# Performance work log

Hardware: AMD Instinct MI355X
Metric: run time of the kernel (lower is better)

## Reference

```python
import jax, jax.numpy as jnp
import numpy as np

N_NODES = 50000
N_EDGES = 800000
IN_DIM = 128
OUT_DIM = 64
K_KERNELS = 2
S_ATTEN = 2


def setup_inputs() -> dict:
    key = jax.random.key(0)
    ks = jax.random.split(key, 9)
    return {
        "x": jax.random.normal(ks[0], (N_NODES, IN_DIM), dtype=jnp.float32),
        "support_vals": jax.random.uniform(ks[1], (K_KERNELS, N_EDGES), dtype=jnp.float32),
        "atten_vals": jax.random.uniform(ks[2], (S_ATTEN, N_EDGES), dtype=jnp.float32),
        "W_transform": jax.random.normal(ks[3], (K_KERNELS, IN_DIM, OUT_DIM), dtype=jnp.float32) * 0.05,
        "w_left": jax.random.normal(ks[4], (K_KERNELS, S_ATTEN + 1, OUT_DIM), dtype=jnp.float32) * 0.05,
        "w_right": jax.random.normal(ks[5], (K_KERNELS, S_ATTEN + 1, OUT_DIM), dtype=jnp.float32) * 0.05,
        "W_residual": jax.random.normal(ks[6], (IN_DIM + OUT_DIM, OUT_DIM), dtype=jnp.float32) * 0.05,
        "edge_rows": jax.random.randint(ks[7], (N_EDGES,), 0, N_NODES, dtype=jnp.int64),
        "edge_cols": jax.random.randint(ks[8], (N_EDGES,), 0, N_NODES, dtype=jnp.int64),
    }


def reference(x, support_vals, atten_vals, W_transform, w_left, w_right, W_residual, edge_rows, edge_cols):
    # x: [N, F], edge lists: [E]; all supports share the same sparsity pattern.
    N = x.shape[0]
    K = W_transform.shape[0]
    output = jnp.zeros((N, W_transform.shape[2]), dtype=x.dtype)
    for k in range(K):
        wx = x @ W_transform[k]                       # [N, D]
        al = wx @ w_left[k].T                         # [N, S+1]
        ar = wx @ w_right[k].T                        # [N, S+1]
        # per-support edge values; support i=S uses this kernel's Cheb support
        vals = jnp.concatenate([atten_vals, support_vals[k][None, :]], axis=0)  # [S+1, E]
        # score_e = sum_i (al[row_e,i] + ar[col_e,i]) * vals[i,e]
        scores = jnp.einsum('es,se->e', al[edge_rows] + ar[edge_cols], vals)    # [E]
        # row-wise (segment) softmax over nonzeros, as tf.sparse_softmax
        m = jax.ops.segment_max(scores, edge_rows, num_segments=N)              # [N]
        ex = jnp.exp(scores - m[edge_rows])
        denom = jax.ops.segment_sum(ex, edge_rows, num_segments=N)              # [N]
        probs = ex / denom[edge_rows]                                           # [E]
        # spmm: out[r] = sum_{e: row_e=r} probs_e * wx[col_e]
        output = output + jax.ops.segment_sum(probs[:, None] * wx[edge_cols], edge_rows, num_segments=N)
    # residual projection then elu activation
    output = jnp.concatenate([x, output], axis=-1) @ W_residual
    return jax.nn.elu(output)
```

## Files before the change

### kernel.cpp

```cpp
#include <hip/hip_runtime.h>

#define N_NODES 50000
#define N_EDGES 800000
#define IN_DIM 128
#define OUT_DIM 64
#define NEG_INF (-1e30f)
#define GBLK ((N_NODES + 63) / 64)
#define BSHIFT 7
#define NBUK ((N_NODES + 127) >> 7)
#define EB 1024
#define PREB ((N_EDGES + EB - 1) / EB)
#define NFRAG (3 * 16 + 8)
#define STAGE_CAP 3072

typedef unsigned short ushort_t;
typedef __attribute__((ext_vector_type(8))) short short8;
typedef __attribute__((ext_vector_type(4))) float f32x4;

__device__ __forceinline__ unsigned f2bf(float f) {
    unsigned u = __float_as_uint(f);
    u += 0x7fffu + ((u >> 16) & 1u);
    return u >> 16;
}
__device__ __forceinline__ unsigned rl_u(unsigned v, int i) {
    return __builtin_amdgcn_readlane(v, i);
}
__device__ __forceinline__ float rl_f(float v, int i) {
    return __uint_as_float(__builtin_amdgcn_readlane(__float_as_uint(v), i));
}

__global__ void wpack_kernel(const float* __restrict__ Wt,
                             const float* __restrict__ Wres,
                             ushort_t* __restrict__ Wpack) {
    int idx = blockIdx.x * 256 + threadIdx.x;
    if (idx >= NFRAG * 512) return;
    int f = idx >> 9;
    int within = idx & 511;
    int lane = within >> 3;
    int b = within & 7;
    float val;
    if (f < 48) {
        int mat = f >> 4;
        int ct = (f >> 2) & 3;
        int kc = f & 3;
        int k = kc * 32 + (lane >> 4) * 8 + b;
        int c = ct * 16 + (lane & 15);
        const float* W = (mat < 2) ? (Wt + (size_t)mat * IN_DIM * OUT_DIM) : Wres;
        val = W[(size_t)k * OUT_DIM + c];
    } else {
        int f2 = f - 48;
        int ct = f2 >> 1;
        int kc = f2 & 1;
        int k = kc * 32 + (lane >> 4) * 8 + b;
        int c = ct * 16 + (lane & 15);
        val = Wres[(size_t)(IN_DIM + k) * OUT_DIM + c];
    }
    Wpack[idx] = (ushort_t)f2bf(val);
}

__global__ __launch_bounds__(256) void gemm_kernel(
        const float* __restrict__ x,
        const ushort_t* __restrict__ Wpack,
        const float* __restrict__ wl,
        const float* __restrict__ wr,
        unsigned* __restrict__ wxi,
        float* __restrict__ xres,
        float* __restrict__ al,
        float* __restrict__ ar) {
    int wave = threadIdx.x >> 6;
    int lane = threadIdx.x & 63;
    int lr = lane & 15;
    int lg = lane >> 4;
    int row0 = blockIdx.x * 64 + wave * 16;

    int arow = row0 + lr;
    if (arow >= N_NODES) arow = N_NODES - 1;
    const float* xr = x + (size_t)arow * IN_DIM;
    short8 afrag[4];
#pragma unroll
    for (int kc = 0; kc < 4; ++kc) {
        float4 f0 = *(const float4*)(xr + kc * 32 + lg * 8);
        float4 f1 = *(const float4*)(xr + kc * 32 + lg * 8 + 4);
        short8 a;
        a[0] = (short)f2bf(f0.x); a[1] = (short)f2bf(f0.y);
        a[2] = (short)f2bf(f0.z); a[3] = (short)f2bf(f0.w);
        a[4] = (short)f2bf(f1.x); a[5] = (short)f2bf(f1.y);
        a[6] = (short)f2bf(f1.z); a[7] = (short)f2bf(f1.w);
        afrag[kc] = a;
    }

    f32x4 acc[3][4] = {};
#pragma unroll
    for (int kc = 0; kc < 4; ++kc) {
#pragma unroll
        for (int mat = 0; mat < 3; ++mat) {
#pragma unroll
            for (int ct = 0; ct < 4; ++ct) {
                short8 bfrag = *(const short8*)(
                    Wpack + (size_t)(((mat * 4 + ct) * 4 + kc) << 9) + lane * 8);
                acc[mat][ct] = __builtin_amdgcn_mfma_f32_16x16x32_bf16(
                    afrag[kc], bfrag, acc[mat][ct], 0, 0, 0);
            }
        }
    }

#pragma unroll
    for (int r = 0; r < 4; ++r) {
        int gr = row0 + lg * 4 + r;
        if (gr < N_NODES) {
#pragma unroll
            for (int ct = 0; ct < 4; ++ct) {
                unsigned pk = f2bf(acc[0][ct][r]) | (f2bf(acc[1][ct][r]) << 16);
                wxi[(size_t)gr * OUT_DIM + ct * 16 + lr] = pk;
                xres[(size_t)gr * OUT_DIM + ct * 16 + lr] = acc[2][ct][r];
            }
        }
    }

#pragma unroll
    for (int mat = 0; mat < 2; ++mat) {
#pragma unroll
        for (int s = 0; s < 3; ++s) {
            float wlv[4], wrv[4];
#pragma unroll
            for (int ct = 0; ct < 4; ++ct) {
                wlv[ct] = wl[(size_t)(mat * 3 + s) * OUT_DIM + ct * 16 + lr];
                wrv[ct] = wr[(size_t)(mat * 3 + s) * OUT_DIM + ct * 16 + lr];
            }
#pragma unroll
            for (int r = 0; r < 4; ++r) {
                float pl = 0.f, pr = 0.f;
#pragma unroll
                for (int ct = 0; ct < 4; ++ct) {
                    pl = fmaf(acc[mat][ct][r], wlv[ct], pl);
                    pr = fmaf(acc[mat][ct][r], wrv[ct], pr);
                }
#pragma unroll
                for (int off = 1; off < 16; off <<= 1) {
                    pl += __shfl_xor(pl, off);
                    pr += __shfl_xor(pr, off);
                }
                if (lr == 0) {
                    int gr = row0 + lg * 4 + r;
                    if (gr < N_NODES) {
                        al[(size_t)gr * 6 + mat * 3 + s] = pl;
                        ar[(size_t)gr * 6 + mat * 3 + s] = pr;
                    }
                }
            }
        }
    }
}

__global__ __launch_bounds__(256) void score_sort_kernel(
        const int* __restrict__ rows,
        const int* __restrict__ cols,
        const float* __restrict__ atten,
        const float* __restrict__ support,
        const float* __restrict__ al,
        const float* __restrict__ ar,
        uint4* __restrict__ etmp,
        int* __restrict__ cnt_T,
        int* __restrict__ loff_T) {
    __shared__ int cnt[512];
    __shared__ int cur[512];
    __shared__ int aux[256];
    __shared__ uint4 stage[EB];
    int t = threadIdx.x;
    cnt[t] = 0; cnt[t + 256] = 0;
    __syncthreads();
    int base0 = blockIdx.x * EB;
    int nval = min(EB, N_EDGES - base0);

    int r_[4], c_[4];
    float s0_[4], s1_[4];
#pragma unroll
    for (int i = 0; i < 4; ++i) {
        int e = base0 + i * 256 + t;
        bool v = e < N_EDGES;
        int r = v ? rows[e] : -1;
        int c = v ? cols[e] : 0;
        float sc0 = 0.f, sc1 = 0.f;
        if (v) {
            float a0 = atten[e], a1 = atten[N_EDGES + e];
            float sp0 = support[e], sp1 = support[N_EDGES + e];
            const float* A = al + (size_t)r * 6;
            const float* B = ar + (size_t)c * 6;
            sc0 = (A[0] + B[0]) * a0 + (A[1] + B[1]) * a1 + (A[2] + B[2]) * sp0;
            sc1 = (A[3] + B[3]) * a0 + (A[4] + B[4]) * a1 + (A[5] + B[5]) * sp1;
            atomicAdd(&cnt[r >> BSHIFT], 1);
        }
        r_[i] = r; c_[i] = c; s0_[i] = sc0; s1_[i] = sc1;
    }
    __syncthreads();
    int a0 = cnt[2 * t], a1 = cnt[2 * t + 1];
    int ps = a0 + a1;
    aux[t] = ps;
    __syncthreads();
    int val = ps;
    for (int off = 1; off < 256; off <<= 1) {
        int y = (t >= off) ? aux[t - off] : 0;
        __syncthreads();
        val += y; aux[t] = val;
        __syncthreads();
    }
    int e2 = val - ps;
    cur[2 * t] = e2;
    cur[2 * t + 1] = e2 + a0;
    int b = blockIdx.x;
    if (2 * t < NBUK)     { cnt_T[(2 * t) * PREB + b] = a0;     loff_T[(2 * t) * PREB + b] = e2; }
    if (2 * t + 1 < NBUK) { cnt_T[(2 * t + 1) * PREB + b] = a1; loff_T[(2 * t + 1) * PREB + b] = e2 + a0; }
    __syncthreads();
#pragma unroll
    for (int i = 0; i < 4; ++i) {
        if (r_[i] < 0) continue;
        int pos = atomicAdd(&cur[r_[i] >> BSHIFT], 1);
        uint4 pv;
        pv.x = (unsigned)c_[i] | ((unsigned)(r_[i] & 127) << 16);
        pv.y = __float_as_uint(s0_[i]);
        pv.z = __float_as_uint(s1_[i]);
        pv.w = 0u;
        stage[pos] = pv;
    }
    __syncthreads();
    for (int i = t; i < nval; i += 256)
        etmp[(size_t)base0 + i] = stage[i];
}

__global__ void colscan_kernel(const int* __restrict__ cnt_T,
                               int* __restrict__ btot) {
    __shared__ int sh[256];
    int k = blockIdx.x, t = threadIdx.x;
    int s = 0;
    for (int b = t; b < PREB; b += 256) s += cnt_T[(size_t)k * PREB + b];
    sh[t] = s;
    __syncthreads();
    for (int off = 128; off > 0; off >>= 1) {
        if (t < off) sh[t] += sh[t + off];
        __syncthreads();
    }
    if (t == 0) btot[k] = sh[0];
}

__global__ __launch_bounds__(256) void sortb_kernel(
        const int* __restrict__ cnt_T,
        const int* __restrict__ loff_T,
        const int* __restrict__ btot,
        const uint4* __restrict__ etmp,
        uint4* __restrict__ edata,
        int* __restrict__ row_ptr) {
    __shared__ uint4 stage[STAGE_CAP];
    __shared__ int rpos[PREB + 2];
    __shared__ int lloff[PREB];
    __shared__ int aux[256];
    __shared__ int bb[512];
    __shared__ int hist[128], rcur[128];
    int k = blockIdx.x, t = threadIdx.x;

    bb[t] = (t < NBUK) ? btot[t] : 0;
    bb[t + 256] = (t + 256 < NBUK) ? btot[t + 256] : 0;
    __syncthreads();
    int a0 = bb[2 * t], a1 = bb[2 * t + 1];
    int ps = a0 + a1;
    aux[t] = ps;
    __syncthreads();
    int val = ps;
    for (int off = 1; off < 256; off <<= 1) {
        int y = (t >= off) ? aux[t - off] : 0;
        __syncthreads();
        val += y; aux[t] = val;
        __syncthreads();
    }
    bb[2 * t] = val - ps;
    bb[2 * t + 1] = val - ps + a0;
    __syncthreads();
    int base = bb[k];

    for (int b = t; b < PREB; b += 256) {
        rpos[b] = cnt_T[(size_t)k * PREB + b];
        lloff[b] = loff_T[(size_t)k * PREB + b];
    }
    if (t < 128) hist[t] = 0;
    __syncthreads();
    int v[4];
    int idx4 = 4 * t;
#pragma unroll
    for (int i = 0; i < 4; ++i) v[i] = (idx4 + i < PREB) ? rpos[idx4 + i] : 0;
    __syncthreads();
    int s = 0;
#pragma unroll
    for (int i = 0; i < 4; ++i) { int tmp = v[i]; v[i] = s; s += tmp; }
    aux[t] = s;
    __syncthreads();
    int tv = s;
    for (int off = 1; off < 256; off <<= 1) {
        int y = (t >= off) ? aux[t - off] : 0;
        __syncthreads();
        tv += y; aux[t] = tv;
        __syncthreads();
    }
    int ofs = tv - s;
#pragma unroll
    for (int i = 0; i < 4; ++i)
        if (idx4 + i <= PREB) rpos[idx4 + i] = ofs + v[i];
    __syncthreads();
    int nb = rpos[PREB];

    for (int j = t; j < nb; j += 256) {
        int lo = 0, hi = PREB - 1;
        while (lo < hi) { int mid = (lo + hi + 1) >> 1; if (rpos[mid] <= j) lo = mid; else hi = mid - 1; }
        uint4 rec = etmp[(size_t)lo * EB + lloff[lo] + (j - rpos[lo])];
        if (j < STAGE_CAP) stage[j] = rec;
        atomicAdd(&hist[(rec.x >> 16) & 127], 1);
    }
    __syncthreads();
    int hv = (t < 128) ? hist[t] : 0;
    aux[t] = hv;
    __syncthreads();
    int hval = hv;
    for (int off = 1; off < 128; off <<= 1) {
        int y = (t >= off && t < 128) ? aux[t - off] : 0;
        __syncthreads();
        hval += y; aux[t] = hval;
        __syncthreads();
    }
    if (t < 128) {
        rcur[t] = hval - hv;
        int row = (k << BSHIFT) + t;
        if (row < N_NODES) row_ptr[row] = base + hval - hv;
    }
    if (k == NBUK - 1 && t == 0) row_ptr[N_NODES] = N_EDGES;
    __syncthreads();
    for (int j = t; j < nb; j += 256) {
        uint4 rec;
        if (j < STAGE_CAP) rec = stage[j];
        else {
            int lo = 0, hi = PREB - 1;
            while (lo < hi) { int mid = (lo + hi + 1) >> 1; if (rpos[mid] <= j) lo = mid; else hi = mid - 1; }
            rec = etmp[(size_t)lo * EB + lloff[lo] + (j - rpos[lo])];
        }
        int rl = (rec.x >> 16) & 127;
        int dst = atomicAdd(&rcur[rl], 1);
        edata[(size_t)base + dst] = rec;
    }
}

__global__ void attn_kernel(const int* __restrict__ row_ptr,
                            const uint4* __restrict__ edata,
                            const unsigned* __restrict__ wxi,
                            float* __restrict__ aacc) {
    int wid = blockIdx.x * 4 + (threadIdx.x >> 6);
    if (wid >= N_NODES) return;
    int lane = threadIdx.x & 63;
    int beg = row_ptr[wid], end = row_ptr[wid + 1];
    int deg = end - beg;
    float a = 0.f;

    if (deg > 0 && deg <= 64) {
        bool valid = lane < deg;
        uint4 ed = edata[valid ? beg + lane : beg];
        unsigned c = ed.x & 0xFFFFu;
        float sc0 = valid ? __uint_as_float(ed.y) : NEG_INF;
        float sc1 = valid ? __uint_as_float(ed.z) : NEG_INF;
        float m0 = sc0, m1 = sc1;
#pragma unroll
        for (int off = 32; off > 0; off >>= 1) {
            m0 = fmaxf(m0, __shfl_xor(m0, off));
            m1 = fmaxf(m1, __shfl_xor(m1, off));
        }
        float e0 = valid ? __expf(sc0 - m0) : 0.f;
        float e1 = valid ? __expf(sc1 - m1) : 0.f;
        float l0 = e0, l1 = e1;
#pragma unroll
        for (int off = 32; off > 0; off >>= 1) {
            l0 += __shfl_xor(l0, off);
            l1 += __shfl_xor(l1, off);
        }
        float p0 = e0 / l0;
        float p1 = e1 / l1;
        float a0 = 0.f, a1 = 0.f, a2 = 0.f, a3 = 0.f;
        int i = 0;
        for (; i + 4 <= deg; i += 4) {
            unsigned c0 = rl_u(c, i),     c1 = rl_u(c, i + 1);
            unsigned c2 = rl_u(c, i + 2), c3 = rl_u(c, i + 3);
            unsigned v0 = wxi[(size_t)c0 * OUT_DIM + lane];
            unsigned v1 = wxi[(size_t)c1 * OUT_DIM + lane];
            unsigned v2 = wxi[(size_t)c2 * OUT_DIM + lane];
            unsigned v3 = wxi[(size_t)c3 * OUT_DIM + lane];
            a0 = fmaf(rl_f(p0, i),     __uint_as_float(v0 << 16), a0);
            a0 = fmaf(rl_f(p1, i),     __uint_as_float(v0 & 0xffff0000u), a0);
            a1 = fmaf(rl_f(p0, i + 1), __uint_as_float(v1 << 16), a1);
            a1 = fmaf(rl_f(p1, i + 1), __uint_as_float(v1 & 0xffff0000u), a1);
            a2 = fmaf(rl_f(p0, i + 2), __uint_as_float(v2 << 16), a2);
            a2 = fmaf(rl_f(p1, i + 2), __uint_as_float(v2 & 0xffff0000u), a2);
            a3 = fmaf(rl_f(p0, i + 3), __uint_as_float(v3 << 16), a3);
            a3 = fmaf(rl_f(p1, i + 3), __uint_as_float(v3 & 0xffff0000u), a3);
        }
        for (; i < deg; ++i) {
            unsigned ci = rl_u(c, i);
            unsigned v = wxi[(size_t)ci * OUT_DIM + lane];
            a0 = fmaf(rl_f(p0, i), __uint_as_float(v << 16), a0);
            a0 = fmaf(rl_f(p1, i), __uint_as_float(v & 0xffff0000u), a0);
        }
        a = (a0 + a1) + (a2 + a3);
    } else if (deg > 64) {
        float m0 = NEG_INF, l0 = 0.f, m1 = NEG_INF, l1 = 0.f;
        for (int base = beg; base < end; base += 64) {
            int pos = base + lane;
            bool valid = pos < end;
            uint4 ed = edata[valid ? pos : beg];
            float sc0 = valid ? __uint_as_float(ed.y) : NEG_INF;
            float sc1 = valid ? __uint_as_float(ed.z) : NEG_INF;
            float cm0 = sc0, cm1 = sc1;
#pragma unroll
            for (int off = 32; off > 0; off >>= 1) {
                cm0 = fmaxf(cm0, __shfl_xor(cm0, off));
                cm1 = fmaxf(cm1, __shfl_xor(cm1, off));
            }
            float mn0 = fmaxf(m0, cm0), mn1 = fmaxf(m1, cm1);
            float e0 = valid ? __expf(sc0 - mn0) : 0.f;
            float e1 = valid ? __expf(sc1 - mn1) : 0.f;
#pragma unroll
            for (int off = 32; off > 0; off >>= 1) {
                e0 += __shfl_xor(e0, off);
                e1 += __shfl_xor(e1, off);
            }
            l0 = l0 * __expf(m0 - mn0) + e0;
            l1 = l1 * __expf(m1 - mn1) + e1;
            m0 = mn0; m1 = mn1;
        }
        float inv0 = 1.f / l0, inv1 = 1.f / l1;
        for (int base = beg; base < end; base += 64) {
            int pos = base + lane;
            bool valid = pos < end;
            uint4 ed = edata[valid ? pos : beg];
            unsigned c = ed.x & 0xFFFFu;
            float p0 = valid ? __expf(__uint_as_float(ed.y) - m0) * inv0 : 0.f;
            float p1 = valid ? __expf(__uint_as_float(ed.z) - m1) * inv1 : 0.f;
            int cnt = min(64, end - base);
            for (int i = 0; i < cnt; ++i) {
                unsigned ci = rl_u(c, i);
                unsigned v = wxi[(size_t)ci * OUT_DIM + lane];
                a = fmaf(rl_f(p0, i), __uint_as_float(v << 16), a);
                a = fmaf(rl_f(p1, i), __uint_as_float(v & 0xffff0000u), a);
            }
        }
    }
    aacc[(size_t)wid * OUT_DIM + lane] = a;
}

__global__ __launch_bounds__(256) void resid_kernel(
        const float* __restrict__ aacc,
        const float* __restrict__ xres,
        const ushort_t* __restrict__ Wpack,
        float* __restrict__ out) {
    int wave = threadIdx.x >> 6;
    int lane = threadIdx.x & 63;
    int lr = lane & 15;
    int lg = lane >> 4;
    int row0 = blockIdx.x * 64 + wave * 16;
    int arow = row0 + lr;
    if (arow >= N_NODES) arow = N_NODES - 1;
    const float* ap = aacc + (size_t)arow * OUT_DIM;
    short8 af[2];
#pragma unroll
    for (int kc = 0; kc < 2; ++kc) {
        float4 f0 = *(const float4*)(ap + kc * 32 + lg * 8);
        float4 f1 = *(const float4*)(ap + kc * 32 + lg * 8 + 4);
        short8 a;
        a[0] = (short)f2bf(f0.x); a[1] = (short)f2bf(f0.y);
        a[2] = (short)f2bf(f0.z); a[3] = (short)f2bf(f0.w);
        a[4] = (short)f2bf(f1.x); a[5] = (short)f2bf(f1.y);
        a[6] = (short)f2bf(f1.z); a[7] = (short)f2bf(f1.w);
        af[kc] = a;
    }
    f32x4 acc4[4] = {};
#pragma unroll
    for (int kc = 0; kc < 2; ++kc) {
#pragma unroll
        for (int ct = 0; ct < 4; ++ct) {
            short8 bfrag = *(const short8*)(
                Wpack + (size_t)((48 + ct * 2 + kc) << 9) + lane * 8);
            acc4[ct] = __builtin_amdgcn_mfma_f32_16x16x32_bf16(
                af[kc], bfrag, acc4[ct], 0, 0, 0);
        }
    }
#pragma unroll
    for (int r = 0; r < 4; ++r) {
        int gr = row0 + lg * 4 + r;
        if (gr < N_NODES) {
#pragma unroll
            for (int ct = 0; ct < 4; ++ct) {
                float v = acc4[ct][r] + xres[(size_t)gr * OUT_DIM + ct * 16 + lr];
                out[(size_t)gr * OUT_DIM + ct * 16 + lr] = (v > 0.f) ? v : expm1f(v);
            }
        }
    }
}

extern "C" void kernel_launch(void* const* d_in, const int* in_sizes, int n_in,
                              void* d_out, int out_size, void* d_ws, size_t ws_size,
                              hipStream_t stream) {
    const float* x       = (const float*)d_in[0];
    const float* support = (const float*)d_in[1];
    const float* atten   = (const float*)d_in[2];
    const float* Wt      = (const float*)d_in[3];
    const float* wl      = (const float*)d_in[4];
    const float* wr      = (const float*)d_in[5];
    const float* Wres    = (const float*)d_in[6];
    const int*   rows    = (const int*)d_in[7];
    const int*   cols    = (const int*)d_in[8];
    float* out = (float*)d_out;

    unsigned* wxi   = (unsigned*)d_ws;
    float* xres     = (float*)(wxi + (size_t)N_NODES * OUT_DIM);
    float* al       = xres + (size_t)N_NODES * OUT_DIM;
    float* ar       = al + (size_t)N_NODES * 6;
    uint4* etmp     = (uint4*)(ar + (size_t)N_NODES * 6);
    uint4* edata    = etmp + (size_t)N_EDGES;
    int*   row_ptr  = (int*)(edata + (size_t)N_EDGES);
    int*   cnt_T    = row_ptr + N_NODES + 4;
    int*   loff_T   = cnt_T + (size_t)NBUK * PREB;
    int*   btot     = loff_T + (size_t)NBUK * PREB;
    ushort_t* Wpack = (ushort_t*)(btot + NBUK + 4);
    float* aacc     = (float*)etmp;

    wpack_kernel<<<(NFRAG * 512 + 255) / 256, 256, 0, stream>>>(Wt, Wres, Wpack);
    gemm_kernel<<<GBLK, 256, 0, stream>>>(x, Wpack, wl, wr, wxi, xres, al, ar);
    score_sort_kernel<<<PREB, 256, 0, stream>>>(
        rows, cols, atten, support, al, ar, etmp, cnt_T, loff_T);
    colscan_kernel<<<NBUK, 256, 0, stream>>>(cnt_T, btot);
    sortb_kernel<<<NBUK, 256, 0, stream>>>(
        cnt_T, loff_T, btot, etmp, edata, row_ptr);
    attn_kernel<<<(N_NODES + 3) / 4, 256, 0, stream>>>(
        row_ptr, edata, wxi, aacc);
    resid_kernel<<<GBLK, 256, 0, stream>>>(aacc, xres, Wpack, out);
}
```

Before: 153.7 us.

## Interleave bucket counts, chunk sortb gather, widen attn unroll, store bf16 aggregate

Bucket counts and local offsets are packed into one block-major uint2 array, so score_sort writes are coalesced and a single load fetches both values. sortb now walks each pre-block's contiguous run instead of binary-searching per element. attn unrolls the neighbor gather to 8 independent loads with 8 accumulators for more memory-level parallelism. The aggregated output is stored as bf16 so resid reads half the bytes and skips conversion. The trade-offs are strided column reads in colscan/sortb, per-thread serial loops with uneven work in sortb, and higher register pressure in attn.

```diff
diff --git a/kernel.cpp b/kernel.cpp
--- a/kernel.cpp
+++ b/kernel.cpp
@@ -8,6 +8,7 @@
 #define GBLK ((N_NODES + 63) / 64)
 #define BSHIFT 7
 #define NBUK ((N_NODES + 127) >> 7)
+#define NBUKP 392
 #define EB 1024
 #define PREB ((N_EDGES + EB - 1) / EB)
 #define NFRAG (3 * 16 + 8)
@@ -160,8 +161,7 @@
         const float* __restrict__ al,
         const float* __restrict__ ar,
         uint4* __restrict__ etmp,
-        int* __restrict__ cnt_T,
-        int* __restrict__ loff_T) {
+        uint2* __restrict__ cl) {
     __shared__ int cnt[512];
     __shared__ int cur[512];
     __shared__ int aux[256];
@@ -207,9 +207,9 @@
     int e2 = val - ps;
     cur[2 * t] = e2;
     cur[2 * t + 1] = e2 + a0;
-    int b = blockIdx.x;
-    if (2 * t < NBUK)     { cnt_T[(2 * t) * PREB + b] = a0;     loff_T[(2 * t) * PREB + b] = e2; }
-    if (2 * t + 1 < NBUK) { cnt_T[(2 * t + 1) * PREB + b] = a1; loff_T[(2 * t + 1) * PREB + b] = e2 + a0; }
+    size_t cb = (size_t)blockIdx.x * NBUKP;
+    if (2 * t < NBUK)     cl[cb + 2 * t]     = make_uint2((unsigned)a0, (unsigned)e2);
+    if (2 * t + 1 < NBUK) cl[cb + 2 * t + 1] = make_uint2((unsigned)a1, (unsigned)(e2 + a0));
     __syncthreads();
 #pragma unroll
     for (int i = 0; i < 4; ++i) {
@@ -227,12 +227,12 @@
         etmp[(size_t)base0 + i] = stage[i];
 }
 
-__global__ void colscan_kernel(const int* __restrict__ cnt_T,
+__global__ void colscan_kernel(const uint2* __restrict__ cl,
                                int* __restrict__ btot) {
     __shared__ int sh[256];
     int k = blockIdx.x, t = threadIdx.x;
     int s = 0;
-    for (int b = t; b < PREB; b += 256) s += cnt_T[(size_t)k * PREB + b];
+    for (int b = t; b < PREB; b += 256) s += (int)cl[(size_t)b * NBUKP + k].x;
     sh[t] = s;
     __syncthreads();
     for (int off = 128; off > 0; off >>= 1) {
@@ -243,8 +243,7 @@
 }
 
 __global__ __launch_bounds__(256) void sortb_kernel(
-        const int* __restrict__ cnt_T,
-        const int* __restrict__ loff_T,
+        const uint2* __restrict__ cl,
         const int* __restrict__ btot,
         const uint4* __restrict__ etmp,
         uint4* __restrict__ edata,
@@ -277,8 +276,9 @@
     int base = bb[k];
 
     for (int b = t; b < PREB; b += 256) {
-        rpos[b] = cnt_T[(size_t)k * PREB + b];
-        lloff[b] = loff_T[(size_t)k * PREB + b];
+        uint2 v2 = cl[(size_t)b * NBUKP + k];
+        rpos[b] = (int)v2.x;
+        lloff[b] = (int)v2.y;
     }
     if (t < 128) hist[t] = 0;
     __syncthreads();
@@ -306,12 +306,17 @@
     __syncthreads();
     int nb = rpos[PREB];
 
-    for (int j = t; j < nb; j += 256) {
-        int lo = 0, hi = PREB - 1;
-        while (lo < hi) { int mid = (lo + hi + 1) >> 1; if (rpos[mid] <= j) lo = mid; else hi = mid - 1; }
-        uint4 rec = etmp[(size_t)lo * EB + lloff[lo] + (j - rpos[lo])];
-        if (j < STAGE_CAP) stage[j] = rec;
-        atomicAdd(&hist[(rec.x >> 16) & 127], 1);
+    for (int b = t; b < PREB; b += 256) {
+        int s0 = rpos[b];
+        int n = rpos[b + 1] - s0;
+        int lo = lloff[b];
+        const uint4* src = etmp + (size_t)b * EB + lo;
+        for (int i = 0; i < n; ++i) {
+            uint4 rec = src[i];
+            int j = s0 + i;
+            if (j < STAGE_CAP) stage[j] = rec;
+            atomicAdd(&hist[(rec.x >> 16) & 127], 1);
+        }
     }
     __syncthreads();
     int hv = (t < 128) ? hist[t] : 0;
@@ -348,7 +353,7 @@
 __global__ void attn_kernel(const int* __restrict__ row_ptr,
                             const uint4* __restrict__ edata,
                             const unsigned* __restrict__ wxi,
-                            float* __restrict__ aacc) {
+                            ushort_t* __restrict__ aacc) {
     int wid = blockIdx.x * 4 + (threadIdx.x >> 6);
     if (wid >= N_NODES) return;
     int lane = threadIdx.x & 63;
@@ -378,31 +383,28 @@
         }
         float p0 = e0 / l0;
         float p1 = e1 / l1;
-        float a0 = 0.f, a1 = 0.f, a2 = 0.f, a3 = 0.f;
+        float acc8[8] = {};
         int i = 0;
-        for (; i + 4 <= deg; i += 4) {
-            unsigned c0 = rl_u(c, i),     c1 = rl_u(c, i + 1);
-            unsigned c2 = rl_u(c, i + 2), c3 = rl_u(c, i + 3);
-            unsigned v0 = wxi[(size_t)c0 * OUT_DIM + lane];
-            unsigned v1 = wxi[(size_t)c1 * OUT_DIM + lane];
-            unsigned v2 = wxi[(size_t)c2 * OUT_DIM + lane];
-            unsigned v3 = wxi[(size_t)c3 * OUT_DIM + lane];
-            a0 = fmaf(rl_f(p0, i),     __uint_as_float(v0 << 16), a0);
-            a0 = fmaf(rl_f(p1, i),     __uint_as_float(v0 & 0xffff0000u), a0);
-            a1 = fmaf(rl_f(p0, i + 1), __uint_as_float(v1 << 16), a1);
-            a1 = fmaf(rl_f(p1, i + 1), __uint_as_float(v1 & 0xffff0000u), a1);
-            a2 = fmaf(rl_f(p0, i + 2), __uint_as_float(v2 << 16), a2);
-            a2 = fmaf(rl_f(p1, i + 2), __uint_as_float(v2 & 0xffff0000u), a2);
-            a3 = fmaf(rl_f(p0, i + 3), __uint_as_float(v3 << 16), a3);
-            a3 = fmaf(rl_f(p1, i + 3), __uint_as_float(v3 & 0xffff0000u), a3);
+        for (; i + 8 <= deg; i += 8) {
+            unsigned cc[8], vv[8];
+#pragma unroll
+            for (int j = 0; j < 8; ++j) cc[j] = rl_u(c, i + j);
+#pragma unroll
+            for (int j = 0; j < 8; ++j) vv[j] = wxi[(size_t)cc[j] * OUT_DIM + lane];
+#pragma unroll
+            for (int j = 0; j < 8; ++j) {
+                acc8[j] = fmaf(rl_f(p0, i + j), __uint_as_float(vv[j] << 16), acc8[j]);
+                acc8[j] = fmaf(rl_f(p1, i + j), __uint_as_float(vv[j] & 0xffff0000u), acc8[j]);
+            }
         }
         for (; i < deg; ++i) {
             unsigned ci = rl_u(c, i);
             unsigned v = wxi[(size_t)ci * OUT_DIM + lane];
-            a0 = fmaf(rl_f(p0, i), __uint_as_float(v << 16), a0);
-            a0 = fmaf(rl_f(p1, i), __uint_as_float(v & 0xffff0000u), a0);
-        }
-        a = (a0 + a1) + (a2 + a3);
+            acc8[0] = fmaf(rl_f(p0, i), __uint_as_float(v << 16), acc8[0]);
+            acc8[0] = fmaf(rl_f(p1, i), __uint_as_float(v & 0xffff0000u), acc8[0]);
+        }
+        a = ((acc8[0] + acc8[1]) + (acc8[2] + acc8[3]))
+          + ((acc8[4] + acc8[5]) + (acc8[6] + acc8[7]));
     } else if (deg > 64) {
         float m0 = NEG_INF, l0 = 0.f, m1 = NEG_INF, l1 = 0.f;
         for (int base = beg; base < end; base += 64) {
@@ -446,11 +448,11 @@
             }
         }
     }
-    aacc[(size_t)wid * OUT_DIM + lane] = a;
+    aacc[(size_t)wid * OUT_DIM + lane] = (ushort_t)f2bf(a);
 }
 
 __global__ __launch_bounds__(256) void resid_kernel(
-        const float* __restrict__ aacc,
+        const ushort_t* __restrict__ aacc,
         const float* __restrict__ xres,
         const ushort_t* __restrict__ Wpack,
         float* __restrict__ out) {
@@ -461,19 +463,11 @@
     int row0 = blockIdx.x * 64 + wave * 16;
     int arow = row0 + lr;
     if (arow >= N_NODES) arow = N_NODES - 1;
-    const float* ap = aacc + (size_t)arow * OUT_DIM;
+    const ushort_t* ap = aacc + (size_t)arow * OUT_DIM;
     short8 af[2];
 #pragma unroll
-    for (int kc = 0; kc < 2; ++kc) {
-        float4 f0 = *(const float4*)(ap + kc * 32 + lg * 8);
-        float4 f1 = *(const float4*)(ap + kc * 32 + lg * 8 + 4);
-        short8 a;
-        a[0] = (short)f2bf(f0.x); a[1] = (short)f2bf(f0.y);
-        a[2] = (short)f2bf(f0.z); a[3] = (short)f2bf(f0.w);
-        a[4] = (short)f2bf(f1.x); a[5] = (short)f2bf(f1.y);
-        a[6] = (short)f2bf(f1.z); a[7] = (short)f2bf(f1.w);
-        af[kc] = a;
-    }
+    for (int kc = 0; kc < 2; ++kc)
+        af[kc] = *(const short8*)(ap + kc * 32 + lg * 8);
     f32x4 acc4[4] = {};
 #pragma unroll
     for (int kc = 0; kc < 2; ++kc) {
@@ -519,19 +513,18 @@
     uint4* etmp     = (uint4*)(ar + (size_t)N_NODES * 6);
     uint4* edata    = etmp + (size_t)N_EDGES;
     int*   row_ptr  = (int*)(edata + (size_t)N_EDGES);
-    int*   cnt_T    = row_ptr + N_NODES + 4;
-    int*   loff_T   = cnt_T + (size_t)NBUK * PREB;
-    int*   btot     = loff_T + (size_t)NBUK * PREB;
+    uint2* cl       = (uint2*)(row_ptr + N_NODES + 4);
+    int*   btot     = (int*)(cl + (size_t)PREB * NBUKP);
     ushort_t* Wpack = (ushort_t*)(btot + NBUK + 4);
-    float* aacc     = (float*)etmp;
+    ushort_t* aacc  = (ushort_t*)etmp;
 
     wpack_kernel<<<(NFRAG * 512 + 255) / 256, 256, 0, stream>>>(Wt, Wres, Wpack);
     gemm_kernel<<<GBLK, 256, 0, stream>>>(x, Wpack, wl, wr, wxi, xres, al, ar);
     score_sort_kernel<<<PREB, 256, 0, stream>>>(
-        rows, cols, atten, support, al, ar, etmp, cnt_T, loff_T);
-    colscan_kernel<<<NBUK, 256, 0, stream>>>(cnt_T, btot);
+        rows, cols, atten, support, al, ar, etmp, cl);
+    colscan_kernel<<<NBUK, 256, 0, stream>>>(cl, btot);
     sortb_kernel<<<NBUK, 256, 0, stream>>>(
-        cnt_T, loff_T, btot, etmp, edata, row_ptr);
+        cl, btot, etmp, edata, row_ptr);
     attn_kernel<<<(N_NODES + 3) / 4, 256, 0, stream>>>(
         row_ptr, edata, wxi, aacc);
     resid_kernel<<<GBLK, 256, 0, stream>>>(aacc, xres, Wpack, out);
```

Measured after the change: 140.3 us. 8.7% less time.
